# Optimization experiments

Hardware: AMD Instinct MI355X
Metric: run time of the kernel (lower is better)

The kernel has to match this reference:

```python
import jax, jax.numpy as jnp
import numpy as np


def setup_inputs() -> dict:
    key = jax.random.key(0)
    k1, k2 = jax.random.split(key)
    x = jax.random.normal(k1, (4, 4096, 1024), dtype=jnp.float32)
    codebook = jax.random.normal(k2, (16384, 1024), dtype=jnp.float32)
    return {"x": x, "codebook": codebook}


def reference(x, codebook):
    # Euclidean snap: argmin over pairwise L2 distances, then gather.
    # Squared distances suffice for argmin (monotone transform of cdist p=2).
    x2 = jnp.sum(x * x, axis=-1, keepdims=True)            # [b, n, 1]
    c2 = jnp.sum(codebook * codebook, axis=-1)             # [c]
    xc = jnp.einsum('bnd,cd->bnc', x, codebook)            # [b, n, c]
    d2 = x2 - 2.0 * xc + c2                                # [b, n, c]
    codebook_ids = jnp.argmin(d2, axis=-1)                 # [b, n]
    output = jnp.take(codebook, codebook_ids, axis=0)      # [b, n, d]
    return output
```

## Files before the change

### kernel.cpp

```cpp
#include <hip/hip_runtime.h>
#include <hip/hip_bf16.h>
#include <hip/hip_fp8.h>
#include <stdint.h>

#define NROWS  16384
#define NCODES 16384
#define DIM    1024
#define NT     16
#define MARGIN_Q 514

typedef float f32x4   __attribute__((ext_vector_type(4)));
typedef float f32x16  __attribute__((ext_vector_type(16)));
typedef int   i32x4   __attribute__((ext_vector_type(4)));
typedef int   i32x8   __attribute__((ext_vector_type(8)));
typedef short bf16x8  __attribute__((ext_vector_type(8)));
typedef unsigned char uchar;

__device__ __forceinline__ ushort f2bf(float f) {
  uint32_t u = __float_as_uint(f);
  uint32_t r = u + 0x7FFFu + ((u >> 16) & 1u);
  return (ushort)(r >> 16);
}
__device__ __forceinline__ int imin(int a, int b){ return a < b ? a : b; }
__device__ __forceinline__ int imax(int a, int b){ return a < b ? b : a; }
__device__ __forceinline__ int packKey32(float s, int idx) {
  int q = (int)rintf(s * 16.0f);
  return q * 16384 + idx;
}

#define GLDS16(gp, lp) \
  __builtin_amdgcn_global_load_lds((const __attribute__((address_space(1))) void*)(gp), \
                                   (__attribute__((address_space(3))) void*)(lp), 16, 0, 0)

__device__ __forceinline__ void sbar() {
  asm volatile("" ::: "memory");
  __builtin_amdgcn_s_barrier();
  asm volatile("" ::: "memory");
}

__global__ __launch_bounds__(256) void c2_kernel(const float* __restrict__ cb,
                                                 float* __restrict__ c2) {
  const int code = blockIdx.x;
  const int t = threadIdx.x, lane = t & 63, wid = t >> 6;
  f32x4 v = *(const f32x4*)(cb + (size_t)code * DIM + t * 4);
  float s = v[0]*v[0] + v[1]*v[1] + v[2]*v[2] + v[3]*v[3];
  #pragma unroll
  for (int off = 32; off; off >>= 1) s += __shfl_down(s, off);
  __shared__ float part[4];
  if (lane == 0) part[wid] = s;
  __syncthreads();
  if (t == 0) c2[code] = part[0] + part[1] + part[2] + part[3];
}

__global__ __launch_bounds__(256) void convert_fp8_mxc(const float* __restrict__ src,
                                                       uchar* __restrict__ dst) {
  const int c  = blockIdx.x * 256 + threadIdx.x;
  const int q   = c & 1023;
  const int kt  = (c >> 10) & 15;
  const int m   = c >> 14;
  const int r   = q >> 2;
  const int j   = q & 3;
  const float* s = src + (size_t)(m * 256 + r) * DIM + kt * 64 + j * 16;
  uint64_t lo = 0, hi = 0;
  #pragma unroll
  for (int jj = 0; jj < 8; ++jj) {
    __hip_fp8_e4m3 a(s[jj]);
    __hip_fp8_e4m3 b(s[jj + 8]);
    lo |= (uint64_t)a.__x << (8 * jj);
    hi |= (uint64_t)b.__x << (8 * jj);
  }
  const int st = r >> 5;
  const int h  = j & 1;
  const int l  = (r & 31) + 32 * (j >> 1);
  const size_t wch = (size_t)(m * 16 + kt) * 1024 + st * 128 + h * 64 + l;
  uint64_t* o = (uint64_t*)(dst + wch * 16);
  o[0] = lo; o[1] = hi;
}

#define STAGE_A(BUF, KT) do {                                                     \
    GLDS16(ga + (KT)*16384,        &lsA[BUF][w*1024]);                            \
    GLDS16(ga + (KT)*16384 + 8192, &lsA[BUF][w*1024 + 8192]);                     \
  } while (0)
#define STAGE_B(BUF, KT) do {                                                     \
    GLDS16(gb + (KT)*16384,        &lsB[BUF][w*1024]);                            \
    GLDS16(gb + (KT)*16384 + 8192, &lsB[BUF][w*1024 + 8192]);                     \
  } while (0)

#define RD_A(BUF) do {                                                            \
    _Pragma("unroll")                                                             \
    for (int mi_ = 0; mi_ < 4; ++mi_) {                                           \
      i32x4 lo_ = *(const i32x4*)(Abase[BUF] + mi_ * 2048);                       \
      i32x4 hi_ = *(const i32x4*)(Abase[BUF] + mi_ * 2048 + 1024);                \
      _Pragma("unroll")                                                           \
      for (int j_ = 0; j_ < 4; ++j_) { aF[mi_][j_] = lo_[j_]; aF[mi_][4+j_] = hi_[j_]; } \
    } } while (0)
#define RD_B(BUF) do {                                                            \
    _Pragma("unroll")                                                             \
    for (int nb_ = 0; nb_ < 2; ++nb_) {                                           \
      i32x4 lo_ = *(const i32x4*)(Bbase[BUF] + nb_ * 2048);                       \
      i32x4 hi_ = *(const i32x4*)(Bbase[BUF] + nb_ * 2048 + 1024);                \
      _Pragma("unroll")                                                           \
      for (int j_ = 0; j_ < 4; ++j_) { bF[nb_][j_] = lo_[j_]; bF[nb_][4+j_] = hi_[j_]; } \
    } } while (0)

#define MMA_ALL do {                                                              \
    __builtin_amdgcn_s_setprio(1);                                                \
    _Pragma("unroll")                                                             \
    for (int mi_ = 0; mi_ < 4; ++mi_) {                                           \
      _Pragma("unroll")                                                           \
      for (int nb_ = 0; nb_ < 2; ++nb_)                                           \
        asm("v_mfma_f32_32x32x64_f8f6f4 %0, %1, %2, %3"                           \
            : "=a"(acc[mi_][nb_])                                                 \
            : "v"(aF[mi_]), "v"(bF[nb_]), "0"(acc[mi_][nb_]));                    \
    }                                                                             \
    __builtin_amdgcn_s_setprio(0);                                                \
  } while (0)

#define G4  asm volatile("s_waitcnt vmcnt(4)" ::: "memory")
#define G0  asm volatile("s_waitcnt vmcnt(0)" ::: "memory")
#define NOG do {} while (0)

#define TILE(KT, CUR, NXT, DOST, GUARD) do {                                      \
    if (DOST) { STAGE_A(NXT, (KT) + 2); STAGE_B(NXT, (KT) + 2); }                 \
    RD_B(CUR);                                                                    \
    RD_A(CUR);                                                                    \
    MMA_ALL;                                                                      \
    asm volatile("s_waitcnt lgkmcnt(0)" ::: "memory");                            \
    GUARD;                                                                        \
    sbar();                                                                       \
  } while (0)

__global__ __launch_bounds__(512, 2) void snap_gemm256(const uchar* __restrict__ xs,
                                                       const uchar* __restrict__ cs,
                                                       const float* __restrict__ c2,
                                                       int* __restrict__ cand) {
  __shared__ uchar lsA[3][16384];
  __shared__ uchar lsB[3][16384];

  const int t    = threadIdx.x;
  const int lane = t & 63;
  const int w    = t >> 6;
  const int wm   = w >> 2;
  const int wn   = w & 3;

  const int bid = blockIdx.x;
  const int swz = (bid & 7) * 512 + (bid >> 3);
  const int bm  = swz & 63;
  const int bn  = swz >> 6;

  const uchar* ga = xs + (size_t)bm * 16 * 16384 + w * 1024 + lane * 16;
  const uchar* gb = cs + (size_t)bn * 16 * 16384 + w * 1024 + lane * 16;

  const uchar* Abase[3]; const uchar* Bbase[3];
  #pragma unroll
  for (int b = 0; b < 3; ++b) {
    Abase[b] = &lsA[b][wm * 8192 + lane * 16];
    Bbase[b] = &lsB[b][wn * 4096 + lane * 16];
  }

  f32x16 acc[4][2];
  #pragma unroll
  for (int mi = 0; mi < 4; ++mi)
    #pragma unroll
    for (int nb = 0; nb < 2; ++nb)
      #pragma unroll
      for (int r = 0; r < 16; ++r)
        acc[mi][nb][r] = 0.f;

  i32x8 aF[4], bF[2];

  STAGE_A(0, 0); STAGE_B(0, 0);
  STAGE_A(1, 1); STAGE_B(1, 1);
  G4;
  sbar();

  TILE(0 , 0, 2, 1, G4);
  TILE(1 , 1, 0, 1, G4);
  TILE(2 , 2, 1, 1, G4);
  TILE(3 , 0, 2, 1, G4);
  TILE(4 , 1, 0, 1, G4);
  TILE(5 , 2, 1, 1, G4);
  TILE(6 , 0, 2, 1, G4);
  TILE(7 , 1, 0, 1, G4);
  TILE(8 , 2, 1, 1, G4);
  TILE(9 , 0, 2, 1, G4);
  TILE(10, 1, 0, 1, G4);
  TILE(11, 2, 1, 1, G4);
  TILE(12, 0, 2, 1, G4);
  TILE(13, 1, 0, 1, G4);
  TILE(14, 2, 1, 0, G0);
  TILE(15, 0, 1, 0, NOG);

  __syncthreads();

  int* red = (int*)&lsA[0][0];
  const int colb = bn * 256 + wn * 64 + (lane & 31);
  const float c2v0 = c2[colb];
  const float c2v1 = c2[colb + 32];
  const int rbase = wm * 128 + 4 * (lane >> 5);

  #pragma unroll
  for (int mi = 0; mi < 4; ++mi) {
    #pragma unroll
    for (int reg = 0; reg < 16; ++reg) {
      int ka = packKey32(fmaf(-2.0f, acc[mi][0][reg], c2v0), colb);
      int kb = packKey32(fmaf(-2.0f, acc[mi][1][reg], c2v1), colb + 32);
      int k1 = imin(ka, kb), k2 = imax(ka, kb);
      #pragma unroll
      for (int m = 1; m < 32; m <<= 1) {
        int o1 = __shfl_xor(k1, m);
        int o2 = __shfl_xor(k2, m);
        int n1 = imin(k1, o1);
        int n2 = imin(imax(k1, o1), imin(k2, o2));
        k1 = n1; k2 = n2;
      }
      if ((lane & 31) == 0) {
        int row = rbase + mi * 32 + (reg & 3) + 8 * (reg >> 2);
        red[(wn * 256 + row) * 2 + 0] = k1;
        red[(wn * 256 + row) * 2 + 1] = k2;
      }
    }
  }
  __syncthreads();

  if (t < 256) {
    int k1 = red[(0 * 256 + t) * 2 + 0];
    int k2 = red[(0 * 256 + t) * 2 + 1];
    #pragma unroll
    for (int q = 1; q < 4; ++q) {
      int p1 = red[(q * 256 + t) * 2 + 0];
      int p2 = red[(q * 256 + t) * 2 + 1];
      int n1 = imin(k1, p1);
      int n2 = imin(imax(k1, p1), imin(k2, p2));
      k1 = n1; k2 = n2;
    }
    size_t o = (size_t)(bm * 256 + t) * 128 + (size_t)bn * 2;
    cand[o]     = k1;
    cand[o + 1] = k2;
  }
}

__global__ __launch_bounds__(256) void snap_gemm_slow(const float* __restrict__ x,
                                                      const float* __restrict__ cb,
                                                      const float* __restrict__ c2,
                                                      int* __restrict__ cand) {
  __shared__ ushort lsA[2][8192];
  __shared__ ushort lsB[2][8192];
  __shared__ int redbuf[2][128][2];

  const int t    = threadIdx.x;
  const int lane = t & 63;
  const int wid  = t >> 6;
  const int wm   = wid & 1;
  const int wn   = wid >> 1;
  const int l15  = lane & 15;
  const int kgrp = lane >> 4;

  const int bm = blockIdx.x & 127;
  const int bn = blockIdx.x >> 7;
  const int rowBase = bm * 128;
  const int colBase = bn * 128;

  const float* aptr[4];
  const float* bptr[4];
  int ldsOff[4];
  #pragma unroll
  for (int i = 0; i < 4; ++i) {
    int pc = t + 256 * i;
    int row = pc >> 3;
    int g = (pc & 7) ^ (row & 7);
    aptr[i] = x  + (size_t)(rowBase + row) * DIM + g * 8;
    bptr[i] = cb + (size_t)(colBase + row) * DIM + g * 8;
    ldsOff[i] = pc * 8;
  }

  f32x4 acc[4][4];
  #pragma unroll
  for (int mi = 0; mi < 4; ++mi)
    #pragma unroll
    for (int ni = 0; ni < 4; ++ni)
      acc[mi][ni] = (f32x4){0.f, 0.f, 0.f, 0.f};

  auto STAGE = [&](int buf, int kt) {
    const int kOff = kt * 64;
    #pragma unroll
    for (int i = 0; i < 4; ++i) {
      f32x4 a0 = *(const f32x4*)(aptr[i] + kOff);
      f32x4 a1 = *(const f32x4*)(aptr[i] + kOff + 4);
      f32x4 b0 = *(const f32x4*)(bptr[i] + kOff);
      f32x4 b1 = *(const f32x4*)(bptr[i] + kOff + 4);
      bf16x8 pa, pb;
      #pragma unroll
      for (int j = 0; j < 4; ++j) {
        pa[j]     = (short)f2bf(a0[j]);
        pa[j + 4] = (short)f2bf(a1[j]);
        pb[j]     = (short)f2bf(b0[j]);
        pb[j + 4] = (short)f2bf(b1[j]);
      }
      *(bf16x8*)(&lsA[buf][ldsOff[i]]) = pa;
      *(bf16x8*)(&lsB[buf][ldsOff[i]]) = pb;
    }
  };

  STAGE(0, 0);
  __syncthreads();

  for (int kt = 0; kt < DIM / 64; ++kt) {
    const int cur = kt & 1;
    if (kt < DIM / 64 - 1) STAGE(cur ^ 1, kt + 1);

    const ushort* bA = &lsA[cur][0];
    const ushort* bB = &lsB[cur][0];
    #pragma unroll
    for (int ks = 0; ks < 2; ++ks) {
      const int gidx = ks * 4 + kgrp;
      bf16x8 af[4], bfr[4];
      #pragma unroll
      for (int mi = 0; mi < 4; ++mi) {
        int r_ = wm * 64 + mi * 16 + l15;
        af[mi] = *(const bf16x8*)(bA + (r_ * 8 + (gidx ^ (r_ & 7))) * 8);
      }
      #pragma unroll
      for (int ni = 0; ni < 4; ++ni) {
        int c_ = wn * 64 + ni * 16 + l15;
        bfr[ni] = *(const bf16x8*)(bB + (c_ * 8 + (gidx ^ (c_ & 7))) * 8);
      }
      #pragma unroll
      for (int mi = 0; mi < 4; ++mi)
        #pragma unroll
        for (int ni = 0; ni < 4; ++ni)
          acc[mi][ni] = __builtin_amdgcn_mfma_f32_16x16x32_bf16(af[mi], bfr[ni], acc[mi][ni], 0, 0, 0);
    }
    __syncthreads();
  }

  float c2v[4];
  int   colv[4];
  #pragma unroll
  for (int ni = 0; ni < 4; ++ni) {
    colv[ni] = colBase + wn * 64 + ni * 16 + l15;
    c2v[ni]  = c2[colv[ni]];
  }

  #pragma unroll
  for (int mi = 0; mi < 4; ++mi) {
    #pragma unroll
    for (int r = 0; r < 4; ++r) {
      int a = packKey32(fmaf(-2.0f, acc[mi][0][r], c2v[0]), colv[0]);
      int b = packKey32(fmaf(-2.0f, acc[mi][1][r], c2v[1]), colv[1]);
      int c = packKey32(fmaf(-2.0f, acc[mi][2][r], c2v[2]), colv[2]);
      int d = packKey32(fmaf(-2.0f, acc[mi][3][r], c2v[3]), colv[3]);
      int lo1 = imin(a, b), hi1 = imax(a, b);
      int lo2 = imin(c, d), hi2 = imax(c, d);
      int k1 = imin(lo1, lo2);
      int k2 = imin(imax(lo1, lo2), imin(hi1, hi2));
      #pragma unroll
      for (int m = 1; m < 16; m <<= 1) {
        int o1 = __shfl_xor(k1, m);
        int o2 = __shfl_xor(k2, m);
        int n1 = imin(k1, o1);
        int n2 = imin(imax(k1, o1), imin(k2, o2));
        k1 = n1; k2 = n2;
      }
      if (l15 == 0) {
        int rl = wm * 64 + mi * 16 + kgrp * 4 + r;
        redbuf[wn][rl][0] = k1;
        redbuf[wn][rl][1] = k2;
      }
    }
  }
  __syncthreads();

  if (t < 128) {
    int a1 = redbuf[0][t][0], a2 = redbuf[0][t][1];
    int b1 = redbuf[1][t][0], b2 = redbuf[1][t][1];
    int m1 = imin(a1, b1);
    int m2 = imin(imax(a1, b1), imin(a2, b2));
    size_t o = (size_t)(rowBase + t) * 256 + (size_t)bn * 2;
    cand[o]     = m1;
    cand[o + 1] = m2;
  }
}

__global__ __launch_bounds__(256) void rerank(const float* __restrict__ x,
                                              const float* __restrict__ cb,
                                              const int* __restrict__ cand,
                                              int* __restrict__ bestidx,
                                              int poolN) {
  const int row = blockIdx.x;
  const int t = threadIdx.x, lane = t & 63, wid = t >> 6;
  __shared__ int    smin[4];
  __shared__ int    gshared;
  __shared__ double dpart[4];
  __shared__ int    cnt;
  __shared__ int    list[64];

  int my = (t < poolN) ? cand[(size_t)row * poolN + t] : 0x7FFFFFFF;
  int k = my;
  #pragma unroll
  for (int off = 32; off; off >>= 1) k = imin(k, __shfl_down(k, off));
  if (lane == 0) smin[wid] = k;
  if (t == 0) cnt = 0;
  __syncthreads();
  if (t == 0) {
    int g = smin[0];
    for (int i = 1; i < 4; ++i) g = imin(g, smin[i]);
    gshared = g;
  }
  __syncthreads();

  const int gq = gshared >> 14;
  if ((my >> 14) <= gq + MARGIN_Q) {
    int p = atomicAdd(&cnt, 1);
    if (p < 64) list[p] = my & 16383;
  }
  __syncthreads();
  int n = cnt; if (n > 64) n = 64;

  uint64_t best = ~0ull;
  const float* xr = x + (size_t)row * DIM;
  for (int i = 0; i < n; ++i) {
    const int cidx = list[i];
    const float* cr = cb + (size_t)cidx * DIM;
    double p = 0.0;
    #pragma unroll
    for (int j = 0; j < 4; ++j) {
      int d = t + 256 * j;
      double diff = (double)xr[d] - (double)cr[d];
      p += diff * diff;
    }
    #pragma unroll
    for (int off = 32; off; off >>= 1) p += __shfl_down(p, off);
    if (lane == 0) dpart[wid] = p;
    __syncthreads();
    if (t == 0) {
      double d2 = dpart[0] + dpart[1] + dpart[2] + dpart[3];
      uint64_t bits = (uint64_t)__double_as_longlong(d2);
      uint64_t key = (bits & ~0x3FFFull) | (uint32_t)cidx;
      if (key < best) best = key;
    }
    __syncthreads();
  }
  if (t == 0) bestidx[row] = (int)(best & 0x3FFFull);
}

__global__ __launch_bounds__(256) void gather_rows(const float* __restrict__ cb,
                                                   const int* __restrict__ bestidx,
                                                   float* __restrict__ out) {
  const int row = blockIdx.x;
  const int idx = bestidx[row];
  f32x4 v = *(const f32x4*)(cb + (size_t)idx * DIM + threadIdx.x * 4);
  *(f32x4*)(out + (size_t)row * DIM + threadIdx.x * 4) = v;
}

extern "C" void kernel_launch(void* const* d_in, const int* in_sizes, int n_in,
                              void* d_out, int out_size, void* d_ws, size_t ws_size,
                              hipStream_t stream) {
  const float* x  = (const float*)d_in[0];
  const float* cb = (const float*)d_in[1];
  float* out = (float*)d_out;

  float* c2      = (float*)d_ws;
  int*   bestidx = (int*)((char*)d_ws + 64 * 1024);

  const size_t candBytes = (size_t)NROWS * 128 * 4;
  const size_t needFast  = 128 * 1024 + candBytes;

  c2_kernel<<<NCODES, 256, 0, stream>>>(cb, c2);

  if (ws_size >= needFast) {
    uchar* xs = (uchar*)d_out;
    uchar* cs = xs + (size_t)NROWS * DIM;
    int* cand = (int*)((char*)d_ws + 128 * 1024);

    convert_fp8_mxc<<<4096, 256, 0, stream>>>(x,  xs);
    convert_fp8_mxc<<<4096, 256, 0, stream>>>(cb, cs);
    snap_gemm256<<<4096, 512, 0, stream>>>(xs, cs, c2, cand);
    rerank<<<NROWS, 256, 0, stream>>>(x, cb, cand, bestidx, 128);
    gather_rows<<<NROWS, 256, 0, stream>>>(cb, bestidx, out);
  } else {
    int* cand = (int*)d_out;
    snap_gemm_slow<<<(NROWS / 128) * (NCODES / 128), 256, 0, stream>>>(x, cb, c2, cand);
    rerank<<<NROWS, 256, 0, stream>>>(x, cb, cand, bestidx, 256);
    gather_rows<<<NROWS, 256, 0, stream>>>(cb, bestidx, out);
  }
}
```

Measured before the change: 629.1 us.

## Switch GEMM K-loop to double-buffered 128-wide K tiles with fewer barriers

Replaces the triple-buffered 64-wide K staging with double-buffered 128-wide K tiles, so each iteration loads twice the data and runs two MFMA rounds per barrier. This halves the number of block barriers and waitcnt points. In exchange, prefetch depth drops from two tiles ahead to one, and every tile waits on vmcnt(0). That can expose global-to-LDS latency that the deeper pipeline used to hide. LDS use grows from 96KB to 128KB per block, which may limit the two-blocks-per-CU launch bound.

```diff
diff --git a/kernel.cpp b/kernel.cpp
--- a/kernel.cpp
+++ b/kernel.cpp
@@ -6,7 +6,6 @@
 #define NROWS  16384
 #define NCODES 16384
 #define DIM    1024
-#define NT     16
 #define MARGIN_Q 514
 
 typedef float f32x4   __attribute__((ext_vector_type(4)));
@@ -77,28 +76,32 @@
   o[0] = lo; o[1] = hi;
 }
 
-#define STAGE_A(BUF, KT) do {                                                     \
-    GLDS16(ga + (KT)*16384,        &lsA[BUF][w*1024]);                            \
-    GLDS16(ga + (KT)*16384 + 8192, &lsA[BUF][w*1024 + 8192]);                     \
+#define STAGE_A(BUF, KT2) do {                                                    \
+    GLDS16(ga + (KT2)*32768,         &lsA[BUF][w*1024]);                          \
+    GLDS16(ga + (KT2)*32768 +  8192, &lsA[BUF][w*1024 +  8192]);                  \
+    GLDS16(ga + (KT2)*32768 + 16384, &lsA[BUF][w*1024 + 16384]);                  \
+    GLDS16(ga + (KT2)*32768 + 24576, &lsA[BUF][w*1024 + 24576]);                  \
   } while (0)
-#define STAGE_B(BUF, KT) do {                                                     \
-    GLDS16(gb + (KT)*16384,        &lsB[BUF][w*1024]);                            \
-    GLDS16(gb + (KT)*16384 + 8192, &lsB[BUF][w*1024 + 8192]);                     \
+#define STAGE_B(BUF, KT2) do {                                                    \
+    GLDS16(gb + (KT2)*32768,         &lsB[BUF][w*1024]);                          \
+    GLDS16(gb + (KT2)*32768 +  8192, &lsB[BUF][w*1024 +  8192]);                  \
+    GLDS16(gb + (KT2)*32768 + 16384, &lsB[BUF][w*1024 + 16384]);                  \
+    GLDS16(gb + (KT2)*32768 + 24576, &lsB[BUF][w*1024 + 24576]);                  \
   } while (0)
 
-#define RD_A(BUF) do {                                                            \
+#define RD_A(BUF, H) do {                                                         \
     _Pragma("unroll")                                                             \
     for (int mi_ = 0; mi_ < 4; ++mi_) {                                           \
-      i32x4 lo_ = *(const i32x4*)(Abase[BUF] + mi_ * 2048);                       \
-      i32x4 hi_ = *(const i32x4*)(Abase[BUF] + mi_ * 2048 + 1024);                \
+      i32x4 lo_ = *(const i32x4*)(Abase[BUF] + (H)*16384 + mi_ * 2048);           \
+      i32x4 hi_ = *(const i32x4*)(Abase[BUF] + (H)*16384 + mi_ * 2048 + 1024);    \
       _Pragma("unroll")                                                           \
       for (int j_ = 0; j_ < 4; ++j_) { aF[mi_][j_] = lo_[j_]; aF[mi_][4+j_] = hi_[j_]; } \
     } } while (0)
-#define RD_B(BUF) do {                                                            \
+#define RD_B(BUF, H) do {                                                         \
     _Pragma("unroll")                                                             \
     for (int nb_ = 0; nb_ < 2; ++nb_) {                                           \
-      i32x4 lo_ = *(const i32x4*)(Bbase[BUF] + nb_ * 2048);                       \
-      i32x4 hi_ = *(const i32x4*)(Bbase[BUF] + nb_ * 2048 + 1024);                \
+      i32x4 lo_ = *(const i32x4*)(Bbase[BUF] + (H)*16384 + nb_ * 2048);           \
+      i32x4 hi_ = *(const i32x4*)(Bbase[BUF] + (H)*16384 + nb_ * 2048 + 1024);    \
       _Pragma("unroll")                                                           \
       for (int j_ = 0; j_ < 4; ++j_) { bF[nb_][j_] = lo_[j_]; bF[nb_][4+j_] = hi_[j_]; } \
     } } while (0)
@@ -116,14 +119,16 @@
     __builtin_amdgcn_s_setprio(0);                                                \
   } while (0)
 
-#define G4  asm volatile("s_waitcnt vmcnt(4)" ::: "memory")
 #define G0  asm volatile("s_waitcnt vmcnt(0)" ::: "memory")
 #define NOG do {} while (0)
 
-#define TILE(KT, CUR, NXT, DOST, GUARD) do {                                      \
-    if (DOST) { STAGE_A(NXT, (KT) + 2); STAGE_B(NXT, (KT) + 2); }                 \
-    RD_B(CUR);                                                                    \
-    RD_A(CUR);                                                                    \
+#define TILE(KT2, CUR, NXT, DOST, GUARD) do {                                     \
+    if (DOST) { STAGE_A(NXT, (KT2) + 1); STAGE_B(NXT, (KT2) + 1); }               \
+    RD_B(CUR, 0);                                                                 \
+    RD_A(CUR, 0);                                                                 \
+    MMA_ALL;                                                                      \
+    RD_B(CUR, 1);                                                                 \
+    RD_A(CUR, 1);                                                                 \
     MMA_ALL;                                                                      \
     asm volatile("s_waitcnt lgkmcnt(0)" ::: "memory");                            \
     GUARD;                                                                        \
@@ -134,8 +139,8 @@
                                                        const uchar* __restrict__ cs,
                                                        const float* __restrict__ c2,
                                                        int* __restrict__ cand) {
-  __shared__ uchar lsA[3][16384];
-  __shared__ uchar lsB[3][16384];
+  __shared__ uchar lsA[2][32768];
+  __shared__ uchar lsB[2][32768];
 
   const int t    = threadIdx.x;
   const int lane = t & 63;
@@ -151,9 +156,9 @@
   const uchar* ga = xs + (size_t)bm * 16 * 16384 + w * 1024 + lane * 16;
   const uchar* gb = cs + (size_t)bn * 16 * 16384 + w * 1024 + lane * 16;
 
-  const uchar* Abase[3]; const uchar* Bbase[3];
-  #pragma unroll
-  for (int b = 0; b < 3; ++b) {
+  const uchar* Abase[2]; const uchar* Bbase[2];
+  #pragma unroll
+  for (int b = 0; b < 2; ++b) {
     Abase[b] = &lsA[b][wm * 8192 + lane * 16];
     Bbase[b] = &lsB[b][wn * 4096 + lane * 16];
   }
@@ -170,26 +175,17 @@
   i32x8 aF[4], bF[2];
 
   STAGE_A(0, 0); STAGE_B(0, 0);
-  STAGE_A(1, 1); STAGE_B(1, 1);
-  G4;
+  G0;
   sbar();
 
-  TILE(0 , 0, 2, 1, G4);
-  TILE(1 , 1, 0, 1, G4);
-  TILE(2 , 2, 1, 1, G4);
-  TILE(3 , 0, 2, 1, G4);
-  TILE(4 , 1, 0, 1, G4);
-  TILE(5 , 2, 1, 1, G4);
-  TILE(6 , 0, 2, 1, G4);
-  TILE(7 , 1, 0, 1, G4);
-  TILE(8 , 2, 1, 1, G4);
-  TILE(9 , 0, 2, 1, G4);
-  TILE(10, 1, 0, 1, G4);
-  TILE(11, 2, 1, 1, G4);
-  TILE(12, 0, 2, 1, G4);
-  TILE(13, 1, 0, 1, G4);
-  TILE(14, 2, 1, 0, G0);
-  TILE(15, 0, 1, 0, NOG);
+  TILE(0, 0, 1, 1, G0);
+  TILE(1, 1, 0, 1, G0);
+  TILE(2, 0, 1, 1, G0);
+  TILE(3, 1, 0, 1, G0);
+  TILE(4, 0, 1, 1, G0);
+  TILE(5, 1, 0, 1, G0);
+  TILE(6, 0, 1, 1, G0);
+  TILE(7, 1, 0, 0, NOG);
 
   __syncthreads();
 
```

Measured after the change: 611.1 us. 1.03x faster.
